# Kernel optimization log

Measured on AMD Instinct MI355X. Metric: run time of the kernel, lower is better.

Reference implementation:

```python
import jax, jax.numpy as jnp
import numpy as np
from jax import lax

LONG_EDGE = 1024
MAX_SIZE = 1333.0
STRIDES = (4, 8, 16, 32, 64)
SIZES = (32, 64, 128, 256, 512)
RATIOS = (0.5, 1.0, 2.0)
PRE_NMS_TOPK = 6000
POST_NMS_TOPK = 1000
NMS_THRESH = 0.7
NUM_CH = 256


def _gen_anchors_level(scale, ratios, shape, stride):
    # faithful copy of generate_anchors_keras (numpy, static)
    scales, ratios = np.meshgrid(np.array([scale], dtype=np.float64), np.array(ratios, dtype=np.float64))
    scales = scales.flatten(); ratios = ratios.flatten()
    size_ratios = stride * stride / ratios
    widths = np.round(np.sqrt(size_ratios))
    heights = np.round(widths * ratios)
    widths = widths * (scales / stride)
    heights = heights * (scales / stride)
    shifts_y = np.arange(0, shape[0]) * stride + (stride - 1) / 2
    shifts_x = np.arange(0, shape[1]) * stride + (stride - 1) / 2
    shifts_x, shifts_y = np.meshgrid(shifts_x, shifts_y)
    box_widths, box_centers_x = np.meshgrid(widths, shifts_x)
    box_heights, box_centers_y = np.meshgrid(heights, shifts_y)
    box_centers = np.stack([box_centers_y, box_centers_x], axis=2).reshape([-1, 2])
    box_sizes = np.stack([box_heights, box_widths], axis=2).reshape([-1, 2])
    boxes = np.concatenate([box_centers - 0.5 * (box_sizes - 1), box_centers + 0.5 * (box_sizes - 1)], axis=1)
    boxes[:, [2, 3]] += 1
    return boxes[:, [1, 0, 3, 2]].astype(np.float32)


def all_anchors():
    shapes = [(int(np.ceil(LONG_EDGE / s)),) * 2 for s in STRIDES]
    return np.concatenate([_gen_anchors_level(SIZES[i], RATIOS, shapes[i], STRIDES[i]) for i in range(len(STRIDES))], axis=0)


def conv2d(x, w, b, padding):
    y = lax.conv_general_dilated(x, w, (1, 1), padding, dimension_numbers=('NCHW', 'OIHW', 'NCHW'))
    return y + b[None, :, None, None]


def decode_bbox_target(deltas, anchors):
    # deltas, anchors: [K,4]
    txty, twth = deltas[:, :2], deltas[:, 2:]
    x1y1, x2y2 = anchors[:, :2], anchors[:, 2:]
    waha = x2y2 - x1y1
    xaya = (x2y2 + x1y1) * 0.5
    clipv = jnp.float32(np.log(MAX_SIZE / 16.0))
    wbhb = jnp.exp(jnp.minimum(twth, clipv)) * waha
    xbyb = txty * waha + xaya
    return jnp.concatenate([xbyb - wbhb * 0.5, xbyb + wbhb * 0.5], axis=1)


def clip_boxes(b, h, w):
    # faithful to source: x clamped to window[0]=h, y to window[1]=w
    return jnp.stack([b[:, 0].clip(0.0, h), b[:, 1].clip(0.0, w), b[:, 2].clip(0.0, h), b[:, 3].clip(0.0, w)], 1)


def nms_keep(boxes, thresh):
    # boxes sorted by descending score; greedy NMS over full IoU matrix
    x1, y1, x2, y2 = boxes[:, 0], boxes[:, 1], boxes[:, 2], boxes[:, 3]
    areas = (x2 - x1) * (y2 - y1)
    iw = jnp.clip(jnp.minimum(x2[:, None], x2[None, :]) - jnp.maximum(x1[:, None], x1[None, :]), 0.0)
    ih = jnp.clip(jnp.minimum(y2[:, None], y2[None, :]) - jnp.maximum(y1[:, None], y1[None, :]), 0.0)
    inter = iw * ih
    iou = inter / (areas[:, None] + areas[None, :] - inter)
    n = boxes.shape[0]
    sup = iou > thresh
    idxs = jnp.arange(n)
    def body(i, keep):
        row = sup[i] & (idxs > i)
        return jnp.where(keep[i], keep & ~row, keep)
    return lax.fori_loop(0, n, body, jnp.ones((n,), bool))


def rpn_forward(image, feats, w0, b0, wcls, bcls, wbox, bbox):
    labels, boxes_l = [], []
    for f in feats:
        hidden = jax.nn.relu(conv2d(f, w0, b0, 'SAME'))
        cls = conv2d(hidden, wcls, bcls, 'VALID')   # [1,A,H,W]
        box = conv2d(hidden, wbox, bbox, 'VALID')   # [1,4A,H,W]
        labels.append(jnp.transpose(cls, (0, 2, 3, 1)).reshape(1, -1, 1))
        boxes_l.append(jnp.transpose(box, (0, 2, 3, 1)).reshape(1, -1, 4))
    scores = jnp.concatenate(labels, axis=1)[0, :, 0]          # [N]
    box_logits = jnp.concatenate(boxes_l, axis=1)[0]           # [N,4]
    anchors = jnp.asarray(all_anchors())                       # [N,4]
    k = min(PRE_NMS_TOPK, anchors.shape[0])
    _, order = lax.top_k(scores, k)
    deltas = box_logits[order]
    pre_anch = anchors[order]
    dec = decode_bbox_target(deltas, pre_anch)
    h, w = float(image.shape[2]), float(image.shape[3])
    boxes = clip_boxes(dec, h, w)
    keep = nms_keep(lax.stop_gradient(boxes), NMS_THRESH)
    sel = jnp.argsort(~keep)[:POST_NMS_TOPK]  # stable: kept boxes in score order, then pad slots
    proposals = jnp.where(keep[sel][:, None], boxes[sel], 0.0)
    return proposals


def setup_inputs() -> dict:
    key = jax.random.key(0)
    ks = jax.random.split(key, 9)
    hw = [256, 128, 64, 32, 16]
    inp = {'image': jax.random.normal(ks[0], (1, 3, 1024, 1024), jnp.float32)}
    for i, s in enumerate(hw):
        inp[f'feat{i}'] = jax.random.normal(jax.random.fold_in(ks[1], i), (1, NUM_CH, s, s), jnp.float32)
    inp['w0'] = jax.random.normal(ks[2], (NUM_CH, NUM_CH, 3, 3), jnp.float32) * 0.01
    inp['b0'] = jnp.zeros((NUM_CH,), jnp.float32)
    inp['wcls'] = jax.random.normal(ks[3], (3, NUM_CH, 1, 1), jnp.float32) * 0.01
    inp['bcls'] = jnp.zeros((3,), jnp.float32)
    inp['wbox'] = jax.random.normal(ks[4], (12, NUM_CH, 1, 1), jnp.float32) * 0.01
    inp['bbox'] = jnp.zeros((12,), jnp.float32)
    return inp


def reference(image, feat0, feat1, feat2, feat3, feat4, w0, b0, wcls, bcls, wbox, bbox):
    feats = [feat0, feat1, feat2, feat3, feat4]
    return rpn_forward(image, feats, w0, b0, wcls, bcls, wbox, bbox)
```

## Files before the change

kernel.cpp:

```cpp
#include <hip/hip_runtime.h>
#include <cstdint>

typedef unsigned long long u64;
typedef unsigned int u32;
typedef unsigned short ushort;
typedef __attribute__((ext_vector_type(8))) short short8;
typedef __attribute__((ext_vector_type(4))) float f32x4;

#define A_TOTAL 261888
#define NPIX    87296
#define KTOP    6000
#define KTARGET 7800
#define NWORDS  94
#define CANDMAX 8192
#define NBINS   16384

__device__ __forceinline__ u64 score_key64(double s) {
  u64 u = (u64)__double_as_longlong(s);
  return (u & 0x8000000000000000ULL) ? ~u : (u | 0x8000000000000000ULL);
}
__device__ __forceinline__ u32 key32(float s) {
  u32 u = __float_as_uint(s);
  return (u & 0x80000000u) ? ~u : (u | 0x80000000u);
}
__device__ __forceinline__ ushort f2bf(float f) {
  u32 u = __float_as_uint(f);
  u32 r = (u + 0x7FFFu + ((u >> 16) & 1u)) >> 16;
  return (ushort)r;
}
__device__ __forceinline__ void pix_level(int pix, int& l, int& off) {
  if (pix < 65536)      { l = 0; off = 0; }
  else if (pix < 81920) { l = 1; off = 65536; }
  else if (pix < 86016) { l = 2; off = 81920; }
  else if (pix < 87040) { l = 3; off = 86016; }
  else                  { l = 4; off = 87040; }
}

__global__ void k_prep_w(const float* __restrict__ w0, float* __restrict__ wt,
                         ushort* __restrict__ wkf) {
  int i = blockIdx.x * 256 + threadIdx.x;
  if (i < 256 * 2304) {
    int o = i & 255;
    int ictap = i >> 8;
    float v = w0[o * 2304 + ictap];
    wt[ictap * 256 + o] = v;
    int ic = ictap / 9;
    int tap = ictap - ic * 9;
    int w = o >> 6, mt = (o >> 4) & 3, l15 = o & 15;
    int ch = ic >> 5, kk = ic & 31;
    int l4 = kk >> 3, e = kk & 7;
    int lane = l4 * 16 + l15;
    wkf[((((w * 4 + mt) * 8 + ch) * 9 + tap) << 9) + lane * 8 + e] = f2bf(v);
  }
}

__global__ __launch_bounds__(256, 2) void k_conv_mfma(
    const float* __restrict__ f0, const float* __restrict__ f1,
    const float* __restrict__ f2, const float* __restrict__ f3,
    const float* __restrict__ f4,
    const ushort* __restrict__ wkf, const float* __restrict__ b0,
    const float* __restrict__ wcls, const float* __restrict__ bcls,
    float* __restrict__ scr)
{
  __shared__ ushort xsl[100][40];
  __shared__ float  part[3][64][17];

  int b = blockIdx.x;
  int l, tb;
  if (b < 1024)      { l = 0; tb = b; }
  else if (b < 1280) { l = 1; tb = b - 1024; }
  else if (b < 1344) { l = 2; tb = b - 1280; }
  else if (b < 1360) { l = 3; tb = b - 1344; }
  else               { l = 4; tb = b - 1360; }
  const float* feat = (l == 0) ? f0 : (l == 1) ? f1 : (l == 2) ? f2 : (l == 3) ? f3 : f4;
  int Hh = 256 >> l;
  int HW = Hh * Hh;
  int pixOff = (l == 0) ? 0 : (l == 1) ? 65536 : (l == 2) ? 81920 : (l == 3) ? 86016 : 87040;
  int shl = 5 - l;
  int ty = (tb >> shl) << 3;
  int tx = (tb & ((1 << shl) - 1)) << 3;

  int tid = threadIdx.x;
  int w = tid >> 6;
  int lane = tid & 63;
  int l15 = lane & 15;
  int l4 = lane >> 4;

  f32x4 zz = {0.f, 0.f, 0.f, 0.f};
  f32x4 acc[4][4];
  #pragma unroll
  for (int mt = 0; mt < 4; ++mt)
    #pragma unroll
    for (int tt = 0; tt < 4; ++tt) acc[mt][tt] = zz;

  for (int ch = 0; ch < 8; ++ch) {
    __syncthreads();
    for (int e = tid; e < 3200; e += 256) {
      int icl = e / 100;
      int sp = e - icl * 100;
      int yy = sp / 10;
      int xx = sp - yy * 10;
      int gy = ty + yy - 1, gx = tx + xx - 1;
      float v = 0.f;
      if (gy >= 0 && gy < Hh && gx >= 0 && gx < Hh)
        v = feat[(ch * 32 + icl) * HW + gy * Hh + gx];
      xsl[sp][icl] = f2bf(v);
    }
    __syncthreads();
    #pragma unroll
    for (int tap = 0; tap < 9; ++tap) {
      int dy = tap / 3;
      int dx = tap - dy * 3;
      short8 af[4], bf[4];
      #pragma unroll
      for (int mt = 0; mt < 4; ++mt) {
        int abase = ((((w * 4 + mt) * 8 + ch) * 9 + tap) << 9) + (lane << 3);
        af[mt] = *(const short8*)(wkf + abase);
      }
      #pragma unroll
      for (int tt = 0; tt < 4; ++tt) {
        int p = (tt << 4) + l15;
        int sp = ((p >> 3) + dy) * 10 + (p & 7) + dx;
        bf[tt] = *(const short8*)&xsl[sp][l4 << 3];
      }
      #pragma unroll
      for (int mt = 0; mt < 4; ++mt)
        #pragma unroll
        for (int tt = 0; tt < 4; ++tt)
          acc[mt][tt] = __builtin_amdgcn_mfma_f32_16x16x32_bf16(af[mt], bf[tt], acc[mt][tt], 0, 0, 0);
    }
  }

  float pr[3][4];
  #pragma unroll
  for (int kk = 0; kk < 3; ++kk)
    #pragma unroll
    for (int tt = 0; tt < 4; ++tt) pr[kk][tt] = 0.f;
  #pragma unroll
  for (int mt = 0; mt < 4; ++mt) {
    #pragma unroll
    for (int r = 0; r < 4; ++r) {
      int oc = (w << 6) + (mt << 4) + (l4 << 2) + r;
      float bb = b0[oc];
      float c0 = wcls[oc], c1 = wcls[256 + oc], c2 = wcls[512 + oc];
      #pragma unroll
      for (int tt = 0; tt < 4; ++tt) {
        float v = acc[mt][tt][r] + bb;
        v = v > 0.f ? v : 0.f;
        pr[0][tt] = fmaf(c0, v, pr[0][tt]);
        pr[1][tt] = fmaf(c1, v, pr[1][tt]);
        pr[2][tt] = fmaf(c2, v, pr[2][tt]);
      }
    }
  }
  __syncthreads();
  #pragma unroll
  for (int kk = 0; kk < 3; ++kk)
    #pragma unroll
    for (int tt = 0; tt < 4; ++tt)
      part[kk][(tt << 4) + l15][(w << 2) + l4] = pr[kk][tt];
  __syncthreads();
  if (tid < 192) {
    int kk = tid >> 6;
    int px = tid & 63;
    float s = 0.f;
    #pragma unroll
    for (int q = 0; q < 16; ++q) s += part[kk][px][q];
    int pix = pixOff + (ty + (px >> 3)) * Hh + (tx + (px & 7));
    scr[pix * 3 + kk] = s + bcls[kk];
  }
}

__global__ void k_hist1(const float* __restrict__ scr, u32* __restrict__ bins) {
  __shared__ u32 h[NBINS];
  int tid = threadIdx.x;
  for (int idx = tid; idx < NBINS; idx += 256) h[idx] = 0;
  __syncthreads();
  for (int i = blockIdx.x * 256 + tid; i < A_TOTAL; i += gridDim.x * 256)
    atomicAdd(&h[key32(scr[i]) >> 18], 1u);
  __syncthreads();
  for (int idx = tid; idx < NBINS; idx += 256) {
    u32 v = h[idx];
    if (v) atomicAdd(&bins[idx], v);
  }
}

__global__ void k_scan1(const u32* __restrict__ bins, u32* __restrict__ meta) {
  __shared__ u32 psum[256];
  int tid = threadIdx.x;
  u32 s = 0;
  for (int u = 0; u < 64; ++u) s += bins[tid * 64 + u];
  psum[tid] = s;
  __syncthreads();
  if (tid == 0) {
    u32 run = 0;
    for (int t = 255; t >= 0; --t) { u32 tmp = psum[t]; psum[t] = run; run += tmp; }
  }
  __syncthreads();
  u32 cum = psum[tid];
  if (cum < (u32)KTARGET) {
    for (int u = 63; u >= 0; --u) {
      u32 bv = bins[tid * 64 + u];
      u32 nc = cum + bv;
      if (nc >= (u32)KTARGET) {
        meta[0] = (u32)(tid * 64 + u);
        meta[2] = cum;
        break;
      }
      cum = nc;
    }
  }
}

__global__ void k_hist2(const float* __restrict__ scr, const u32* __restrict__ meta,
                        u32* __restrict__ sub) {
  int i = blockIdx.x * 256 + threadIdx.x;
  if (i < A_TOTAL) {
    u32 k = key32(scr[i]);
    if ((k >> 18) == meta[0]) atomicAdd(&sub[(k >> 10) & 0xFFu], 1u);
  }
}

__global__ void k_scan2(const u32* __restrict__ sub, u32* __restrict__ meta) {
  if (threadIdx.x == 0) {
    u32 b = meta[0];
    u32 c = meta[2];
    u32 T = b << 18;
    for (int u = 255; u >= 0; --u) {
      c += sub[u];
      if (c >= (u32)KTARGET) { T = (b << 18) | ((u32)u << 10); break; }
    }
    meta[3] = (T >= (2u << 10)) ? (T - (2u << 10)) : 0u;
  }
}

__global__ void k_cnt(const float* __restrict__ scr, const u32* __restrict__ meta,
                      u32* __restrict__ blkCnt) {
  __shared__ u32 wc[4];
  int tid = threadIdx.x;
  int i = blockIdx.x * 256 + tid;
  bool q = (i < A_TOTAL) && (key32(scr[i]) >= meta[3]);
  u64 b = __ballot(q);
  if ((tid & 63) == 0) wc[tid >> 6] = (u32)__popcll(b);
  __syncthreads();
  if (tid == 0) blkCnt[blockIdx.x] = wc[0] + wc[1] + wc[2] + wc[3];
}

__global__ __launch_bounds__(1024) void k_scanblk(const u32* __restrict__ blkCnt,
                                                  u32* __restrict__ blkOff,
                                                  u32* __restrict__ meta) {
  __shared__ u32 buf[2][1024];
  int tid = threadIdx.x;
  u32 v = (tid < 1023) ? blkCnt[tid] : 0u;
  buf[0][tid] = v;
  __syncthreads();
  int src = 0;
  for (int d = 1; d < 1024; d <<= 1) {
    u32 t = buf[src][tid] + ((tid >= d) ? buf[src][tid - d] : 0u);
    buf[src ^ 1][tid] = t;
    src ^= 1;
    __syncthreads();
  }
  if (tid < 1023) blkOff[tid] = buf[src][tid] - v;
  if (tid == 0) meta[1] = buf[src][1022];
}

__global__ void k_fill(const float* __restrict__ scr, const u32* __restrict__ meta,
                       const u32* __restrict__ blkOff, u32* __restrict__ candIdx) {
  __shared__ u32 wbase[4];
  int tid = threadIdx.x;
  int lane = tid & 63, wv = tid >> 6;
  int i = blockIdx.x * 256 + tid;
  bool q = (i < A_TOTAL) && (key32(scr[i]) >= meta[3]);
  u64 b = __ballot(q);
  if (lane == 0) wbase[wv] = (u32)__popcll(b);
  __syncthreads();
  if (tid == 0) {
    u32 r = blkOff[blockIdx.x];
    #pragma unroll
    for (int w2 = 0; w2 < 4; ++w2) { u32 t = wbase[w2]; wbase[w2] = r; r += t; }
  }
  __syncthreads();
  if (q) {
    u32 rank = (u32)__popcll(b & ((1ULL << lane) - 1ULL));
    u32 pos = wbase[wv] + rank;
    if (pos < CANDMAX) candIdx[pos] = (u32)i;
  }
}

#define KC 576
__global__ __launch_bounds__(256, 4) void k_rescore(
    const float* __restrict__ f0, const float* __restrict__ f1,
    const float* __restrict__ f2, const float* __restrict__ f3,
    const float* __restrict__ f4,
    const float* __restrict__ wt, const float* __restrict__ b0,
    const float* __restrict__ wcls, const float* __restrict__ bcls,
    const float* __restrict__ wbox, const float* __restrict__ bbox,
    const u32* __restrict__ candIdx, const u32* __restrict__ meta,
    u64* __restrict__ candKey, u32* __restrict__ candPack, double* __restrict__ candDelta)
{
  __shared__ __align__(16) float patch[2][KC][8];
  __shared__ double wavePart[8][5][4];
  __shared__ int sIdx[8], sValid[8], sY[8], sX[8], sW[8], sL[8], sR[8];

  int tid = threadIdx.x;
  int lane = tid & 63;
  int wv = tid >> 6;
  int base = blockIdx.x * 8;
  u32 cnt = meta[1];
  if (cnt > CANDMAX) cnt = CANDMAX;

  if (base >= (int)cnt) {
    if (tid < 8) {
      candKey[base + tid] = 0ULL;
      candPack[base + tid] = 0xFFFFFFFFu;
    }
    return;
  }

  if (tid < 8) {
    int slot = base + tid;
    int v = slot < (int)cnt;
    sValid[tid] = v;
    int aidx = v ? (int)candIdx[slot] : 0;
    sIdx[tid] = aidx;
    int pix = aidx / 3;
    sR[tid] = aidx - pix * 3;
    int l, off;
    pix_level(pix, l, off);
    int W = 256 >> l;
    int idx = pix - off;
    sL[tid] = l;
    sW[tid] = W;
    sY[tid] = idx >> (8 - l);
    sX[tid] = idx & (W - 1);
  }
  __syncthreads();

  auto stage = [&](int c, int pb) {
    for (int t = tid; t < 1536; t += 256) {
      int s = t / 192;
      int rem = t - s * 192;
      int icl = rem / 3;
      int dy = rem - icl * 3;
      int ic = c * 64 + icl;
      float v0 = 0.f, v1 = 0.f, v2 = 0.f;
      if (sValid[s]) {
        int l = sL[s], W = sW[s], y = sY[s], x = sX[s];
        const float* feat = (l == 0) ? f0 : (l == 1) ? f1 : (l == 2) ? f2 : (l == 3) ? f3 : f4;
        int gy = y + dy - 1;
        if (gy >= 0 && gy < W) {
          const float* rowp = feat + ic * W * W + gy * W;
          if (x - 1 >= 0) v0 = rowp[x - 1];
          v1 = rowp[x];
          if (x + 1 < W) v2 = rowp[x + 1];
        }
      }
      int kb = icl * 9 + dy * 3;
      patch[pb][kb + 0][s] = v0;
      patch[pb][kb + 1][s] = v1;
      patch[pb][kb + 2][s] = v2;
    }
  };

  stage(0, 0);
  __syncthreads();

  double h[8];
  #pragma unroll
  for (int s = 0; s < 8; ++s) h[s] = 0.0;

  for (int c = 0; c < 4; ++c) {
    if (c < 3) stage(c + 1, (c + 1) & 1);
    const float* wcol = wt + (c * KC) * 256 + tid;
    const float (*pc)[8] = patch[c & 1];
    for (int kk = 0; kk < KC; ++kk) {
      double wv_ = (double)wcol[(size_t)kk * 256];
      float4 pa = *(const float4*)&pc[kk][0];
      float4 pb2 = *(const float4*)&pc[kk][4];
      h[0] = fma(wv_, (double)pa.x, h[0]);
      h[1] = fma(wv_, (double)pa.y, h[1]);
      h[2] = fma(wv_, (double)pa.z, h[2]);
      h[3] = fma(wv_, (double)pa.w, h[3]);
      h[4] = fma(wv_, (double)pb2.x, h[4]);
      h[5] = fma(wv_, (double)pb2.y, h[5]);
      h[6] = fma(wv_, (double)pb2.z, h[6]);
      h[7] = fma(wv_, (double)pb2.w, h[7]);
    }
    __syncthreads();
  }

  double bb = (double)b0[tid];
  #pragma unroll
  for (int s = 0; s < 8; ++s) {
    double t = h[s] + bb;
    h[s] = t > 0.0 ? t : 0.0;
  }

  for (int s = 0; s < 8; ++s) {
    if (!sValid[s]) continue;
    int r = sR[s];
    double hv = h[s];
    double p0 = (double)wcls[r * 256 + tid] * hv;
    double p1 = (double)wbox[(r * 4 + 0) * 256 + tid] * hv;
    double p2 = (double)wbox[(r * 4 + 1) * 256 + tid] * hv;
    double p3 = (double)wbox[(r * 4 + 2) * 256 + tid] * hv;
    double p4 = (double)wbox[(r * 4 + 3) * 256 + tid] * hv;
    #pragma unroll
    for (int d = 32; d; d >>= 1) {
      p0 += __shfl_xor(p0, d);
      p1 += __shfl_xor(p1, d);
      p2 += __shfl_xor(p2, d);
      p3 += __shfl_xor(p3, d);
      p4 += __shfl_xor(p4, d);
    }
    if (lane == 0) {
      wavePart[s][0][wv] = p0;
      wavePart[s][1][wv] = p1;
      wavePart[s][2][wv] = p2;
      wavePart[s][3][wv] = p3;
      wavePart[s][4][wv] = p4;
    }
  }
  __syncthreads();
  if (tid < 40) {
    int s = tid / 5;
    int k = tid - s * 5;
    int slot = base + s;
    if (sValid[s]) {
      double v = wavePart[s][k][0] + wavePart[s][k][1] + wavePart[s][k][2] + wavePart[s][k][3];
      int r = sR[s];
      if (k == 0) {
        double sc_ = v + (double)bcls[r];
        candKey[slot] = score_key64(sc_);
        candPack[slot] = ((u32)sIdx[s] << 13) | (u32)slot;
      } else {
        candDelta[(size_t)slot * 4 + (k - 1)] = v + (double)bbox[r * 4 + (k - 1)];
      }
    } else if (k == 0) {
      candKey[slot] = 0ULL;
      candPack[slot] = 0xFFFFFFFFu;
    }
  }
}

__global__ __launch_bounds__(256) void k_rank(const u64* __restrict__ candKey,
                                              const u32* __restrict__ candPack,
                                              u32* __restrict__ order) {
  __shared__ u64 fk[1024];
  __shared__ u32 fp[1024];
  __shared__ u32 rsum[32][8];
  int tid = threadIdx.x;
  int c = tid & 31;
  int g = tid >> 5;
  int ci = blockIdx.x * 32 + c;
  u64 mk = candKey[ci];
  u32 mp = candPack[ci];
  u32 cnt = 0;
  for (int chunk = 0; chunk < 8; ++chunk) {
    __syncthreads();
    for (int e = tid; e < 1024; e += 256) {
      fk[e] = candKey[chunk * 1024 + e];
      fp[e] = candPack[chunk * 1024 + e];
    }
    __syncthreads();
    int j0 = g * 128;
    #pragma unroll 4
    for (int j = j0; j < j0 + 128; ++j) {
      u64 kj = fk[j];
      cnt += (kj > mk || (kj == mk && fp[j] < mp)) ? 1u : 0u;
    }
  }
  rsum[c][g] = cnt;
  __syncthreads();
  if (tid < 32) {
    u32 rank = 0;
    #pragma unroll
    for (int q = 0; q < 8; ++q) rank += rsum[tid][q];
    if (rank < (u32)KTOP) order[rank] = mp;
  }
}

__global__ void k_decode(const u32* __restrict__ order, const double* __restrict__ candDelta,
                         double* __restrict__ boxesD) {
  int i = blockIdx.x * 64 + threadIdx.x;
  if (i >= KTOP) return;
  u32 pack = order[i];
  u32 slot = pack & 0x1FFFu;
  u32 a = pack >> 13;
  int pix = (int)(a / 3u);
  int r = (int)(a - (u32)pix * 3u);
  int l, off;
  pix_level(pix, l, off);
  int W = 256 >> l;
  int idx = pix - off;
  int y = idx >> (8 - l);
  int x = idx & (W - 1);
  int s = 4 << l;
  double ratio = (r == 0) ? 0.5 : (r == 1) ? 1.0 : 2.0;
  double wq = rint(sqrt((double)(s * s) / ratio));
  double hq = rint(wq * ratio);
  double Wa = wq * 8.0, Ha = hq * 8.0;
  double cx = (double)x * (double)s + (double)(s - 1) * 0.5;
  double cy = (double)y * (double)s + (double)(s - 1) * 0.5;
  double ax1 = (double)(float)(cx - 0.5 * (Wa - 1.0));
  double ay1 = (double)(float)(cy - 0.5 * (Ha - 1.0));
  double ax2 = (double)(float)(cx + 0.5 * (Wa - 1.0) + 1.0);
  double ay2 = (double)(float)(cy + 0.5 * (Ha - 1.0) + 1.0);
  double tx = candDelta[(size_t)slot * 4 + 0], tyv = candDelta[(size_t)slot * 4 + 1];
  double tw = candDelta[(size_t)slot * 4 + 2], th  = candDelta[(size_t)slot * 4 + 3];
  double wa = ax2 - ax1, ha = ay2 - ay1;
  double xa = (ax1 + ax2) * 0.5, ya = (ay1 + ay2) * 0.5;
  double clipv = (double)(float)log(1333.0 / 16.0);
  double wb = exp(fmin(tw, clipv)) * wa;
  double hb = exp(fmin(th, clipv)) * ha;
  double xb = tx * wa + xa;
  double yb = tyv * ha + ya;
  double bx1 = xb - 0.5 * wb, by1 = yb - 0.5 * hb;
  double bx2 = xb + 0.5 * wb, by2 = yb + 0.5 * hb;
  bx1 = fmin(fmax(bx1, 0.0), 1024.0);
  by1 = fmin(fmax(by1, 0.0), 1024.0);
  bx2 = fmin(fmax(bx2, 0.0), 1024.0);
  by2 = fmin(fmax(by2, 0.0), 1024.0);
  boxesD[(size_t)i * 4 + 0] = bx1;
  boxesD[(size_t)i * 4 + 1] = by1;
  boxesD[(size_t)i * 4 + 2] = bx2;
  boxesD[(size_t)i * 4 + 3] = by2;
}

__global__ void k_mask(const double* __restrict__ boxesD, u64* __restrict__ maskA) {
  __shared__ double cbx[64][4];
  int lane = threadIdx.x;
  int bc = blockIdx.x, br = blockIdx.y;
  if (bc < br) return;
  int ci = bc * 64 + lane;
  if (ci < KTOP) {
    cbx[lane][0] = boxesD[(size_t)ci * 4 + 0];
    cbx[lane][1] = boxesD[(size_t)ci * 4 + 1];
    cbx[lane][2] = boxesD[(size_t)ci * 4 + 2];
    cbx[lane][3] = boxesD[(size_t)ci * 4 + 3];
  } else {
    cbx[lane][0] = -1e30; cbx[lane][1] = -1e30; cbx[lane][2] = -1e30; cbx[lane][3] = -1e30;
  }
  __syncthreads();
  int ri = br * 64 + lane;
  if (ri >= KTOP) return;
  double rx1 = boxesD[(size_t)ri * 4 + 0], ry1 = boxesD[(size_t)ri * 4 + 1];
  double rx2 = boxesD[(size_t)ri * 4 + 2], ry2 = boxesD[(size_t)ri * 4 + 3];
  double ra = (rx2 - rx1) * (ry2 - ry1);
  u64 bits = 0;
  #pragma unroll 4
  for (int j = 0; j < 64; ++j) {
    int cj = bc * 64 + j;
    double iw = fmin(rx2, cbx[j][2]) - fmax(rx1, cbx[j][0]);
    double ih = fmin(ry2, cbx[j][3]) - fmax(ry1, cbx[j][1]);
    iw = fmax(iw, 0.0); ih = fmax(ih, 0.0);
    double inter = iw * ih;
    double ca = (cbx[j][2] - cbx[j][0]) * (cbx[j][3] - cbx[j][1]);
    double iou = inter / (ra + ca - inter);
    if (cj > ri && iou > 0.7) bits |= (1ULL << j);
  }
  maskA[(size_t)ri * NWORDS + bc] = bits;
}

__global__ __launch_bounds__(1024) void k_nms_reduce(const u64* __restrict__ maskA,
                                                     u32* __restrict__ keep) {
  __shared__ u64 rm[NWORDS];
  int tid = threadIdx.x;
  int wv = tid >> 6, lane = tid & 63;
  for (int i = tid; i < NWORDS; i += 1024) rm[i] = 0ULL;
  __syncthreads();
  u64 diagNext = maskA[(size_t)lane * NWORDS + 0];
  int keptTot = 0;
  for (int c = 0; c < NWORDS; ++c) {
    int rows = KTOP - c * 64; if (rows > 64) rows = 64;
    u64 validM = (rows == 64) ? ~0ULL : ((1ULL << rows) - 1ULL);
    size_t rowbase = (size_t)(c * 64 + lane) * NWORDS;
    bool lv = lane < rows;
    int w0i = c + wv;
    u64 v0 = (lv && w0i      < NWORDS) ? maskA[rowbase + w0i]      : 0ULL;
    u64 v1 = (lv && w0i + 16 < NWORDS) ? maskA[rowbase + w0i + 16] : 0ULL;
    u64 v2 = (lv && w0i + 32 < NWORDS) ? maskA[rowbase + w0i + 32] : 0ULL;
    u64 v3 = (lv && w0i + 48 < NWORDS) ? maskA[rowbase + w0i + 48] : 0ULL;
    u64 v4 = (lv && w0i + 64 < NWORDS) ? maskA[rowbase + w0i + 64] : 0ULL;
    u64 v5 = (lv && w0i + 80 < NWORDS) ? maskA[rowbase + w0i + 80] : 0ULL;
    u64 diag = diagNext;
    if (c + 1 < NWORDS) {
      int nrows = KTOP - (c + 1) * 64; if (nrows > 64) nrows = 64;
      diagNext = (lane < nrows) ? maskA[(size_t)((c + 1) * 64 + lane) * NWORDS + (c + 1)] : 0ULL;
    }
    u64 R = rm[c];
    u64 undec = (~R) & validM;
    u64 km = 0;
    while (undec) {
      int j = __builtin_ctzll(undec);
      km |= (1ULL << j);
      u64 dj = (u64)__shfl((unsigned long long)diag, j);
      undec &= ~(dj | (1ULL << j));
    }
    if (wv == 0 && lane < rows) keep[c * 64 + lane] = (u32)((km >> lane) & 1ULL);
    keptTot += (int)__popcll(km);
    if (keptTot >= 1000) {
      for (int i = (c + 1) * 64 + tid; i < KTOP; i += 1024) keep[i] = 0u;
      return;
    }
    u64 sel = ((km >> lane) & 1ULL) ? ~0ULL : 0ULL;
    v0 &= sel; v1 &= sel; v2 &= sel; v3 &= sel; v4 &= sel; v5 &= sel;
    #pragma unroll
    for (int s = 32; s; s >>= 1) {
      v0 |= (u64)__shfl_xor((unsigned long long)v0, s);
      v1 |= (u64)__shfl_xor((unsigned long long)v1, s);
      v2 |= (u64)__shfl_xor((unsigned long long)v2, s);
      v3 |= (u64)__shfl_xor((unsigned long long)v3, s);
      v4 |= (u64)__shfl_xor((unsigned long long)v4, s);
      v5 |= (u64)__shfl_xor((unsigned long long)v5, s);
    }
    if (lane == 0) {
      if (w0i      < NWORDS) rm[w0i]      |= v0;
      if (w0i + 16 < NWORDS) rm[w0i + 16] |= v1;
      if (w0i + 32 < NWORDS) rm[w0i + 32] |= v2;
      if (w0i + 48 < NWORDS) rm[w0i + 48] |= v3;
      if (w0i + 64 < NWORDS) rm[w0i + 64] |= v4;
      if (w0i + 80 < NWORDS) rm[w0i + 80] |= v5;
    }
    __syncthreads();
  }
}

__global__ __launch_bounds__(1024) void k_emit(const u32* __restrict__ keep,
                                               const double* __restrict__ boxesD,
                                               float* __restrict__ out) {
  __shared__ u32 partial[1024];
  __shared__ u32 excl[1024];
  int tid = threadIdx.x;
  for (int j = tid; j < 4000; j += 1024) out[j] = 0.f;
  int base = tid * 6;
  u32 kv[6];
  u32 c = 0;
  #pragma unroll
  for (int u = 0; u < 6; ++u) {
    int j = base + u;
    kv[u] = (j < KTOP) ? keep[j] : 0u;
    c += kv[u];
  }
  partial[tid] = c;
  __syncthreads();
  if (tid == 0) {
    u32 run = 0;
    for (int t = 0; t < 1024; ++t) { excl[t] = run; run += partial[t]; }
  }
  __syncthreads();
  u32 p = excl[tid];
  #pragma unroll
  for (int u = 0; u < 6; ++u) {
    int j = base + u;
    if (j < KTOP && kv[u]) {
      if (p < 1000u) {
        out[p * 4 + 0] = (float)boxesD[(size_t)j * 4 + 0];
        out[p * 4 + 1] = (float)boxesD[(size_t)j * 4 + 1];
        out[p * 4 + 2] = (float)boxesD[(size_t)j * 4 + 2];
        out[p * 4 + 3] = (float)boxesD[(size_t)j * 4 + 3];
      }
      ++p;
    }
  }
}

extern "C" void kernel_launch(void* const* d_in, const int* in_sizes, int n_in,
                              void* d_out, int out_size, void* d_ws, size_t ws_size,
                              hipStream_t stream) {
  const float* f0   = (const float*)d_in[1];
  const float* f1   = (const float*)d_in[2];
  const float* f2   = (const float*)d_in[3];
  const float* f3   = (const float*)d_in[4];
  const float* f4   = (const float*)d_in[5];
  const float* w0   = (const float*)d_in[6];
  const float* b0   = (const float*)d_in[7];
  const float* wcls = (const float*)d_in[8];
  const float* bcls = (const float*)d_in[9];
  const float* wbox = (const float*)d_in[10];
  const float* bbox = (const float*)d_in[11];
  float* out = (float*)d_out;
  char* ws = (char*)d_ws;

  size_t off = 0;
  auto alloc = [&](size_t bytes) { size_t o = off; off += (bytes + 255) & ~(size_t)255; return o; };
  size_t off_scr  = alloc((size_t)A_TOTAL * 4);
  size_t off_wt   = alloc((size_t)256 * 2304 * 4);
  size_t off_wk   = alloc((size_t)256 * 2304 * 2);
  size_t off_ci   = alloc((size_t)CANDMAX * 4);
  size_t off_ck   = alloc((size_t)CANDMAX * 8);
  size_t off_cp   = alloc((size_t)CANDMAX * 4);
  size_t off_cd   = alloc((size_t)CANDMAX * 4 * 8);
  size_t off_box  = alloc((size_t)KTOP * 4 * 8);
  size_t off_ord  = alloc((size_t)KTOP * 4);
  size_t off_keep = alloc((size_t)KTOP * 4);
  size_t off_mask = alloc((size_t)KTOP * NWORDS * 8);
  size_t off_bcnt = alloc((size_t)1024 * 4);
  size_t off_boff = alloc((size_t)1024 * 4);
  size_t off_bins = alloc((size_t)NBINS * 4);
  size_t off_sub  = alloc((size_t)256 * 4);
  size_t off_meta = alloc((size_t)64 * 4);
  size_t off_end  = off;
  (void)in_sizes; (void)n_in; (void)out_size; (void)ws_size;

  float*  scr       = (float*)(ws + off_scr);
  float*  wt        = (float*)(ws + off_wt);
  ushort* wkf       = (ushort*)(ws + off_wk);
  u32*    candIdx   = (u32*)(ws + off_ci);
  u64*    candKey   = (u64*)(ws + off_ck);
  u32*    candPack  = (u32*)(ws + off_cp);
  double* candDelta = (double*)(ws + off_cd);
  double* boxesD    = (double*)(ws + off_box);
  u32*    order     = (u32*)(ws + off_ord);
  u32*    keep      = (u32*)(ws + off_keep);
  u64*    maskA     = (u64*)(ws + off_mask);
  u32*    blkCnt    = (u32*)(ws + off_bcnt);
  u32*    blkOff    = (u32*)(ws + off_boff);
  u32*    bins      = (u32*)(ws + off_bins);
  u32*    sub       = (u32*)(ws + off_sub);
  u32*    meta      = (u32*)(ws + off_meta);

  hipMemsetAsync(ws + off_bins, 0, off_end - off_bins, stream);

  k_prep_w<<<2304, 256, 0, stream>>>(w0, wt, wkf);
  k_conv_mfma<<<1364, 256, 0, stream>>>(f0, f1, f2, f3, f4, wkf, b0, wcls, bcls, scr);
  k_hist1<<<64, 256, 0, stream>>>(scr, bins);
  k_scan1<<<1, 256, 0, stream>>>(bins, meta);
  k_hist2<<<1023, 256, 0, stream>>>(scr, meta, sub);
  k_scan2<<<1, 64, 0, stream>>>(sub, meta);
  k_cnt<<<1023, 256, 0, stream>>>(scr, meta, blkCnt);
  k_scanblk<<<1, 1024, 0, stream>>>(blkCnt, blkOff, meta);
  k_fill<<<1023, 256, 0, stream>>>(scr, meta, blkOff, candIdx);
  k_rescore<<<CANDMAX / 8, 256, 0, stream>>>(f0, f1, f2, f3, f4, wt, b0, wcls, bcls, wbox, bbox,
                                             candIdx, meta, candKey, candPack, candDelta);
  k_rank<<<CANDMAX / 32, 256, 0, stream>>>(candKey, candPack, order);
  k_decode<<<94, 64, 0, stream>>>(order, candDelta, boxesD);
  k_mask<<<dim3(NWORDS, NWORDS), 64, 0, stream>>>(boxesD, maskA);
  k_nms_reduce<<<1, 1024, 0, stream>>>(maskA, keep);
  k_emit<<<1, 1024, 0, stream>>>(keep, boxesD, out);
}
```

Before: 956.3 us.

## Deduplicate fp64 hidden-conv rescore per pixel instead of per anchor

The old rescore computed the fp64 3x3 conv hidden vector once per candidate anchor, so pixels with several candidate anchors repeated the full conv. This adds pixel-level compaction kernels (count, scan, fill with a pixel-to-slot map), computes the hidden vector once per unique candidate pixel into a workspace buffer, and then runs a separate heads kernel that reads that buffer. The trade is three extra small launches and a global round-trip of the fp64 hidden buffer in exchange for fewer heavy fp64 conv evaluations. How much it saves depends on how many candidate anchors share a pixel.

```diff
diff --git a/kernel.cpp b/kernel.cpp
--- a/kernel.cpp
+++ b/kernel.cpp
@@ -13,6 +13,7 @@
 #define KTARGET 7800
 #define NWORDS  94
 #define CANDMAX 8192
+#define PIXMAX  8192
 #define NBINS   16384
 
 __device__ __forceinline__ u64 score_key64(double s) {
@@ -248,7 +249,7 @@
 
 __global__ __launch_bounds__(1024) void k_scanblk(const u32* __restrict__ blkCnt,
                                                   u32* __restrict__ blkOff,
-                                                  u32* __restrict__ meta) {
+                                                  u32* __restrict__ totalOut) {
   __shared__ u32 buf[2][1024];
   int tid = threadIdx.x;
   u32 v = (tid < 1023) ? blkCnt[tid] : 0u;
@@ -262,7 +263,7 @@
     __syncthreads();
   }
   if (tid < 1023) blkOff[tid] = buf[src][tid] - v;
-  if (tid == 0) meta[1] = buf[src][1022];
+  if (tid == 0) totalOut[0] = buf[src][1022];
 }
 
 __global__ void k_fill(const float* __restrict__ scr, const u32* __restrict__ meta,
@@ -288,44 +289,73 @@
   }
 }
 
+__global__ void k_cntP(const float* __restrict__ scr, const u32* __restrict__ meta,
+                       u32* __restrict__ blkCntP) {
+  __shared__ u32 wc[4];
+  int tid = threadIdx.x;
+  int p = blockIdx.x * 256 + tid;
+  bool q = false;
+  if (p < NPIX) {
+    u32 T = meta[3];
+    q = (key32(scr[p * 3 + 0]) >= T) || (key32(scr[p * 3 + 1]) >= T) || (key32(scr[p * 3 + 2]) >= T);
+  }
+  u64 b = __ballot(q);
+  if ((tid & 63) == 0) wc[tid >> 6] = (u32)__popcll(b);
+  __syncthreads();
+  if (tid == 0) blkCntP[blockIdx.x] = wc[0] + wc[1] + wc[2] + wc[3];
+}
+
+__global__ void k_fillP(const float* __restrict__ scr, const u32* __restrict__ meta,
+                        const u32* __restrict__ blkOffP,
+                        u32* __restrict__ pixList, u32* __restrict__ pixMap) {
+  __shared__ u32 wbase[4];
+  int tid = threadIdx.x;
+  int lane = tid & 63, wv = tid >> 6;
+  int p = blockIdx.x * 256 + tid;
+  bool q = false;
+  if (p < NPIX) {
+    u32 T = meta[3];
+    q = (key32(scr[p * 3 + 0]) >= T) || (key32(scr[p * 3 + 1]) >= T) || (key32(scr[p * 3 + 2]) >= T);
+  }
+  u64 b = __ballot(q);
+  if (lane == 0) wbase[wv] = (u32)__popcll(b);
+  __syncthreads();
+  if (tid == 0) {
+    u32 r = blkOffP[blockIdx.x];
+    #pragma unroll
+    for (int w2 = 0; w2 < 4; ++w2) { u32 t = wbase[w2]; wbase[w2] = r; r += t; }
+  }
+  __syncthreads();
+  if (q) {
+    u32 rank = (u32)__popcll(b & ((1ULL << lane) - 1ULL));
+    u32 pos = wbase[wv] + rank;
+    if (pos < PIXMAX) { pixList[pos] = (u32)p; pixMap[p] = pos; }
+  }
+}
+
 #define KC 576
-__global__ __launch_bounds__(256, 4) void k_rescore(
+__global__ __launch_bounds__(256, 4) void k_hidden(
     const float* __restrict__ f0, const float* __restrict__ f1,
     const float* __restrict__ f2, const float* __restrict__ f3,
     const float* __restrict__ f4,
     const float* __restrict__ wt, const float* __restrict__ b0,
-    const float* __restrict__ wcls, const float* __restrict__ bcls,
-    const float* __restrict__ wbox, const float* __restrict__ bbox,
-    const u32* __restrict__ candIdx, const u32* __restrict__ meta,
-    u64* __restrict__ candKey, u32* __restrict__ candPack, double* __restrict__ candDelta)
+    const u32* __restrict__ pixList, const u32* __restrict__ meta,
+    double* __restrict__ hbuf)
 {
   __shared__ __align__(16) float patch[2][KC][8];
-  __shared__ double wavePart[8][5][4];
-  __shared__ int sIdx[8], sValid[8], sY[8], sX[8], sW[8], sL[8], sR[8];
-
-  int tid = threadIdx.x;
-  int lane = tid & 63;
-  int wv = tid >> 6;
+  __shared__ int sValid[8], sY[8], sX[8], sW[8], sL[8];
+
+  int tid = threadIdx.x;
   int base = blockIdx.x * 8;
-  u32 cnt = meta[1];
-  if (cnt > CANDMAX) cnt = CANDMAX;
-
-  if (base >= (int)cnt) {
-    if (tid < 8) {
-      candKey[base + tid] = 0ULL;
-      candPack[base + tid] = 0xFFFFFFFFu;
-    }
-    return;
-  }
+  u32 np = meta[4];
+  if (np > PIXMAX) np = PIXMAX;
+  if (base >= (int)np) return;
 
   if (tid < 8) {
     int slot = base + tid;
-    int v = slot < (int)cnt;
+    int v = slot < (int)np;
     sValid[tid] = v;
-    int aidx = v ? (int)candIdx[slot] : 0;
-    sIdx[tid] = aidx;
-    int pix = aidx / 3;
-    sR[tid] = aidx - pix * 3;
+    int pix = v ? (int)pixList[slot] : 0;
     int l, off;
     pix_level(pix, l, off);
     int W = 256 >> l;
@@ -393,14 +423,53 @@
   double bb = (double)b0[tid];
   #pragma unroll
   for (int s = 0; s < 8; ++s) {
-    double t = h[s] + bb;
-    h[s] = t > 0.0 ? t : 0.0;
-  }
+    if (sValid[s]) {
+      double t = h[s] + bb;
+      hbuf[(size_t)(base + s) * 256 + tid] = t > 0.0 ? t : 0.0;
+    }
+  }
+}
+
+__global__ __launch_bounds__(256, 4) void k_heads(
+    const float* __restrict__ wcls, const float* __restrict__ bcls,
+    const float* __restrict__ wbox, const float* __restrict__ bbox,
+    const u32* __restrict__ candIdx, const u32* __restrict__ pixMap,
+    const u32* __restrict__ meta, const double* __restrict__ hbuf,
+    u64* __restrict__ candKey, u32* __restrict__ candPack, double* __restrict__ candDelta)
+{
+  __shared__ double wavePart[8][5][4];
+  __shared__ int sIdx[8], sValid[8], sR[8], sPS[8];
+  int tid = threadIdx.x;
+  int lane = tid & 63;
+  int wv = tid >> 6;
+  int base = blockIdx.x * 8;
+  u32 cnt = meta[1];
+  if (cnt > CANDMAX) cnt = CANDMAX;
+
+  if (base >= (int)cnt) {
+    if (tid < 8) {
+      candKey[base + tid] = 0ULL;
+      candPack[base + tid] = 0xFFFFFFFFu;
+    }
+    return;
+  }
+
+  if (tid < 8) {
+    int slot = base + tid;
+    int v = slot < (int)cnt;
+    sValid[tid] = v;
+    int aidx = v ? (int)candIdx[slot] : 0;
+    sIdx[tid] = aidx;
+    int pix = aidx / 3;
+    sR[tid] = aidx - pix * 3;
+    sPS[tid] = v ? (int)pixMap[pix] : 0;
+  }
+  __syncthreads();
 
   for (int s = 0; s < 8; ++s) {
     if (!sValid[s]) continue;
     int r = sR[s];
-    double hv = h[s];
+    double hv = hbuf[(size_t)sPS[s] * 256 + tid];
     double p0 = (double)wcls[r * 256 + tid] * hv;
     double p1 = (double)wbox[(r * 4 + 0) * 256 + tid] * hv;
     double p2 = (double)wbox[(r * 4 + 1) * 256 + tid] * hv;
@@ -688,16 +757,21 @@
   size_t off_scr  = alloc((size_t)A_TOTAL * 4);
   size_t off_wt   = alloc((size_t)256 * 2304 * 4);
   size_t off_wk   = alloc((size_t)256 * 2304 * 2);
+  size_t off_hb   = alloc((size_t)PIXMAX * 256 * 8);
   size_t off_ci   = alloc((size_t)CANDMAX * 4);
   size_t off_ck   = alloc((size_t)CANDMAX * 8);
   size_t off_cp   = alloc((size_t)CANDMAX * 4);
   size_t off_cd   = alloc((size_t)CANDMAX * 4 * 8);
+  size_t off_pl   = alloc((size_t)PIXMAX * 4);
+  size_t off_pm   = alloc((size_t)NPIX * 4);
   size_t off_box  = alloc((size_t)KTOP * 4 * 8);
   size_t off_ord  = alloc((size_t)KTOP * 4);
   size_t off_keep = alloc((size_t)KTOP * 4);
   size_t off_mask = alloc((size_t)KTOP * NWORDS * 8);
   size_t off_bcnt = alloc((size_t)1024 * 4);
   size_t off_boff = alloc((size_t)1024 * 4);
+  size_t off_bcp  = alloc((size_t)1024 * 4);
+  size_t off_bop  = alloc((size_t)1024 * 4);
   size_t off_bins = alloc((size_t)NBINS * 4);
   size_t off_sub  = alloc((size_t)256 * 4);
   size_t off_meta = alloc((size_t)64 * 4);
@@ -707,16 +781,21 @@
   float*  scr       = (float*)(ws + off_scr);
   float*  wt        = (float*)(ws + off_wt);
   ushort* wkf       = (ushort*)(ws + off_wk);
+  double* hbuf      = (double*)(ws + off_hb);
   u32*    candIdx   = (u32*)(ws + off_ci);
   u64*    candKey   = (u64*)(ws + off_ck);
   u32*    candPack  = (u32*)(ws + off_cp);
   double* candDelta = (double*)(ws + off_cd);
+  u32*    pixList   = (u32*)(ws + off_pl);
+  u32*    pixMap    = (u32*)(ws + off_pm);
   double* boxesD    = (double*)(ws + off_box);
   u32*    order     = (u32*)(ws + off_ord);
   u32*    keep      = (u32*)(ws + off_keep);
   u64*    maskA     = (u64*)(ws + off_mask);
   u32*    blkCnt    = (u32*)(ws + off_bcnt);
   u32*    blkOff    = (u32*)(ws + off_boff);
+  u32*    blkCntP   = (u32*)(ws + off_bcp);
+  u32*    blkOffP   = (u32*)(ws + off_bop);
   u32*    bins      = (u32*)(ws + off_bins);
   u32*    sub       = (u32*)(ws + off_sub);
   u32*    meta      = (u32*)(ws + off_meta);
@@ -730,10 +809,14 @@
   k_hist2<<<1023, 256, 0, stream>>>(scr, meta, sub);
   k_scan2<<<1, 64, 0, stream>>>(sub, meta);
   k_cnt<<<1023, 256, 0, stream>>>(scr, meta, blkCnt);
-  k_scanblk<<<1, 1024, 0, stream>>>(blkCnt, blkOff, meta);
+  k_scanblk<<<1, 1024, 0, stream>>>(blkCnt, blkOff, meta + 1);
   k_fill<<<1023, 256, 0, stream>>>(scr, meta, blkOff, candIdx);
-  k_rescore<<<CANDMAX / 8, 256, 0, stream>>>(f0, f1, f2, f3, f4, wt, b0, wcls, bcls, wbox, bbox,
-                                             candIdx, meta, candKey, candPack, candDelta);
+  k_cntP<<<1023, 256, 0, stream>>>(scr, meta, blkCntP);
+  k_scanblk<<<1, 1024, 0, stream>>>(blkCntP, blkOffP, meta + 4);
+  k_fillP<<<1023, 256, 0, stream>>>(scr, meta, blkOffP, pixList, pixMap);
+  k_hidden<<<PIXMAX / 8, 256, 0, stream>>>(f0, f1, f2, f3, f4, wt, b0, pixList, meta, hbuf);
+  k_heads<<<CANDMAX / 8, 256, 0, stream>>>(wcls, bcls, wbox, bbox, candIdx, pixMap, meta, hbuf,
+                                           candKey, candPack, candDelta);
   k_rank<<<CANDMAX / 32, 256, 0, stream>>>(candKey, candPack, order);
   k_decode<<<94, 64, 0, stream>>>(order, candDelta, boxesD);
   k_mask<<<dim3(NWORDS, NWORDS), 64, 0, stream>>>(boxesD, maskA);
```

New measurement: 981.3 us. +2.6%, slower.
